# Optimization experiments

Measured on AMD Instinct MI355X. Metric: run time of the kernel, lower is better.

Reference implementation:

```python
import jax, jax.numpy as jnp
import numpy as np

# Binary (sign) weight linear: y = x @ sign(W)^T + b

def _binarize(w):
    # sign with sign(0) mapped to +1, as in typical BinaryLinear impls
    return jnp.where(w >= 0, 1.0, -1.0).astype(w.dtype)

def setup_inputs() -> dict:
    key = jax.random.key(0)
    ks = jax.random.split(key, 7)
    B = 65536
    x = jax.random.normal(ks[0], (B, 28, 28), dtype=jnp.float32)
    W1 = jax.random.normal(ks[1], (1000, 784), dtype=jnp.float32) * 0.05
    b1 = jax.random.normal(ks[2], (1000,), dtype=jnp.float32) * 0.01
    W2 = jax.random.normal(ks[3], (500, 1000), dtype=jnp.float32) * 0.05
    b2 = jax.random.normal(ks[4], (500,), dtype=jnp.float32) * 0.01
    W3 = jax.random.normal(ks[5], (10, 500), dtype=jnp.float32) * 0.05
    b3 = jax.random.normal(ks[6], (10,), dtype=jnp.float32) * 0.01
    return {"x": x, "W1": W1, "b1": b1, "W2": W2, "b2": b2, "W3": W3, "b3": b3}

def reference(x, W1, b1, W2, b2, W3, b3):
    h = x.reshape(x.shape[0], -1)                      # [B, 784]
    h = jnp.maximum(h @ _binarize(W1).T + b1, 0.0)     # [B, 1000]
    h = jnp.maximum(h @ _binarize(W2).T + b2, 0.0)     # [B, 500]
    return h @ _binarize(W3).T + b3                    # [B, 10]
```

## Files before the change

### kernel.cpp

```cpp
#include <hip/hip_runtime.h>
#include <stdint.h>


typedef __attribute__((ext_vector_type(8))) short bf16x8;
typedef __attribute__((ext_vector_type(4))) float f32x4;

typedef const __attribute__((address_space(1))) unsigned int* as1_u32p;
typedef __attribute__((address_space(3))) unsigned int* as3_u32p;

__device__ __forceinline__ void glds16(const void* g, void* l) {
  __builtin_amdgcn_global_load_lds((as1_u32p)g, (as3_u32p)l, 16, 0, 0);
}

__device__ __forceinline__ unsigned short f2bf(float f) {
  union { float f; unsigned u; } c;
  c.f = f;
  unsigned u = c.u;
  u += 0x7FFFu + ((u >> 16) & 1u);
  return (unsigned short)(u >> 16);
}

__global__ void binarize_kernel(const float* __restrict__ src, int Ns, int Ks,
                                short* __restrict__ dst, int Np, int Kp) {
  int idx = blockIdx.x * 256 + threadIdx.x;
  if (idx >= Np * Kp) return;
  int n = idx / Kp;
  int k = idx - n * Kp;
  short v = 0;
  if (n < Ns && k < Ks)
    v = (src[n * Ks + k] >= 0.0f) ? (short)0x3F80 : (short)0xBF80;
  dst[idx] = v;
}

__global__ void convert_x_kernel(const float* __restrict__ X, short* __restrict__ Xp) {
  const int g = blockIdx.x * 256 + threadIdx.x;
  if (g >= 65536 * 100) return;
  const int row = g / 100;
  const int c = (g - row * 100) * 8;
  short tmp[8];
  if (c < 784) {
    const float* s = X + (size_t)row * 784 + c;
    float4 f0 = *(const float4*)s;
    float4 f1 = *(const float4*)(s + 4);
    tmp[0] = (short)f2bf(f0.x); tmp[1] = (short)f2bf(f0.y);
    tmp[2] = (short)f2bf(f0.z); tmp[3] = (short)f2bf(f0.w);
    tmp[4] = (short)f2bf(f1.x); tmp[5] = (short)f2bf(f1.y);
    tmp[6] = (short)f2bf(f1.z); tmp[7] = (short)f2bf(f1.w);
  } else {
#pragma unroll
    for (int i = 0; i < 8; ++i) tmp[i] = 0;
  }
  *(bf16x8*)(Xp + (size_t)row * 800 + c) = *(bf16x8*)(tmp);
}

template <int KP, int NP, int NR>
__global__ __launch_bounds__(256, 2)
void gemm_bb(const short* __restrict__ A, const short* __restrict__ Wb,
             const float* __restrict__ bias, short* __restrict__ Hout) {
  __shared__ short As[128 * 32];
  __shared__ short Bs[128 * 32];

  const int tid = threadIdx.x;
  const int lane = tid & 63;
  const int wave = tid >> 6;
  const int wm = wave >> 1, wn = wave & 1;
  const int l15 = lane & 15;
  const int quad = lane >> 4;
  const int m0 = blockIdx.y * 128;
  const int n0 = blockIdx.x * 128;

  const int sr = wave * 16 + (lane >> 2);
  const int sks = (lane & 3) * 8;
  const short* asrc = A + (size_t)(m0 + sr) * KP + sks;
  const short* bsrc = Wb + (size_t)(n0 + sr) * KP + sks;
  short* adst = As + (wave * 16) * 32;
  short* bdst = Bs + (wave * 16) * 32;

  f32x4 acc[4][4];
#pragma unroll
  for (int i = 0; i < 4; ++i)
#pragma unroll
    for (int j = 0; j < 4; ++j) acc[i][j] = (f32x4){0.f, 0.f, 0.f, 0.f};

  for (int k0 = 0; k0 < KP; k0 += 32) {
    glds16(asrc + k0, adst);
    glds16(asrc + k0 + (size_t)64 * KP, adst + 64 * 32);
    glds16(bsrc + k0, bdst);
    glds16(bsrc + k0 + (size_t)64 * KP, bdst + 64 * 32);
    __syncthreads();

    const short* abase = As + (size_t)(wm * 64 + l15) * 32 + quad * 8;
    const short* bbase = Bs + (size_t)(wn * 64 + l15) * 32 + quad * 8;
    bf16x8 af[4], bfr[4];
#pragma unroll
    for (int i = 0; i < 4; ++i) af[i] = *(const bf16x8*)(abase + i * 16 * 32);
#pragma unroll
    for (int j = 0; j < 4; ++j) bfr[j] = *(const bf16x8*)(bbase + j * 16 * 32);
#pragma unroll
    for (int i = 0; i < 4; ++i)
#pragma unroll
      for (int j = 0; j < 4; ++j)
        acc[i][j] = __builtin_amdgcn_mfma_f32_16x16x32_bf16(af[i], bfr[j], acc[i][j], 0, 0, 0);
    __syncthreads();
  }

#pragma unroll
  for (int j = 0; j < 4; ++j) {
    const int n = n0 + wn * 64 + j * 16 + l15;
    const float bv = (n < NR) ? bias[n] : 0.f;
#pragma unroll
    for (int i = 0; i < 4; ++i) {
      const int mr = m0 + wm * 64 + i * 16 + quad * 4;
#pragma unroll
      for (int r = 0; r < 4; ++r) {
        float v = acc[i][j][r] + bv;
        v = v > 0.f ? v : 0.f;
        Hout[(size_t)(mr + r) * NP + n] = (short)f2bf(v);
      }
    }
  }
}

__global__ __launch_bounds__(256, 2)
void gemm1_fused_kernel(const float* __restrict__ X, const short* __restrict__ Wb,
                        const float* __restrict__ bias, short* __restrict__ H) {
  constexpr int K = 784, KP = 800, NP = 1024, NR = 1000;
  __shared__ short As[128 * 32];
  __shared__ short Bs[128 * 32];

  const int tid = threadIdx.x;
  const int lane = tid & 63;
  const int wave = tid >> 6;
  const int wm = wave >> 1, wn = wave & 1;
  const int l15 = lane & 15;
  const int quad = lane >> 4;
  const int m0 = blockIdx.y * 128;
  const int n0 = blockIdx.x * 128;

  const int ar = tid >> 1;
  const int aks = (tid & 1) * 16;
  const float* xrow = X + (size_t)(m0 + ar) * K;
  short* adst = As + ar * 32 + aks;

  const int br = wave * 16 + (lane >> 2);
  const int bks = (lane & 3) * 8;
  const short* brow0 = Wb + (size_t)(n0 + br) * KP + bks;
  short* bdst = Bs + (wave * 16) * 32;

  f32x4 acc[4][4];
#pragma unroll
  for (int i = 0; i < 4; ++i)
#pragma unroll
    for (int j = 0; j < 4; ++j) acc[i][j] = (f32x4){0.f, 0.f, 0.f, 0.f};

  for (int k0 = 0; k0 < KP; k0 += 32) {
    glds16(brow0 + k0, bdst);
    glds16(brow0 + k0 + (size_t)64 * KP, bdst + 64 * 32);
    short tmp[16];
#pragma unroll
    for (int c = 0; c < 4; ++c) {
      const int kk = k0 + aks + c * 4;
      float4 f;
      if (kk < K)
        f = *(const float4*)(xrow + kk);
      else
        f = make_float4(0.f, 0.f, 0.f, 0.f);
      tmp[c * 4 + 0] = (short)f2bf(f.x);
      tmp[c * 4 + 1] = (short)f2bf(f.y);
      tmp[c * 4 + 2] = (short)f2bf(f.z);
      tmp[c * 4 + 3] = (short)f2bf(f.w);
    }
    *(bf16x8*)(adst) = *(bf16x8*)(tmp);
    *(bf16x8*)(adst + 8) = *(bf16x8*)(tmp + 8);

    __syncthreads();

    const short* abase = As + (size_t)(wm * 64 + l15) * 32 + quad * 8;
    const short* bbase = Bs + (size_t)(wn * 64 + l15) * 32 + quad * 8;
    bf16x8 af[4], bfr[4];
#pragma unroll
    for (int i = 0; i < 4; ++i) af[i] = *(const bf16x8*)(abase + i * 16 * 32);
#pragma unroll
    for (int j = 0; j < 4; ++j) bfr[j] = *(const bf16x8*)(bbase + j * 16 * 32);
#pragma unroll
    for (int i = 0; i < 4; ++i)
#pragma unroll
      for (int j = 0; j < 4; ++j)
        acc[i][j] = __builtin_amdgcn_mfma_f32_16x16x32_bf16(af[i], bfr[j], acc[i][j], 0, 0, 0);
    __syncthreads();
  }

#pragma unroll
  for (int j = 0; j < 4; ++j) {
    const int n = n0 + wn * 64 + j * 16 + l15;
    const float bv = (n < NR) ? bias[n] : 0.f;
#pragma unroll
    for (int i = 0; i < 4; ++i) {
      const int mr = m0 + wm * 64 + i * 16 + quad * 4;
#pragma unroll
      for (int r = 0; r < 4; ++r) {
        float v = acc[i][j][r] + bv;
        v = v > 0.f ? v : 0.f;
        H[(size_t)(mr + r) * NP + n] = (short)f2bf(v);
      }
    }
  }
}

__global__ __launch_bounds__(256, 2)
void gemm3_kernel(const short* __restrict__ Hin, const short* __restrict__ Wb,
                  const float* __restrict__ bias, float* __restrict__ Out) {
  constexpr int KP = 512;
  constexpr int BSTRIDE = 520;
  __shared__ short As[128 * 32];
  __shared__ short Bs[16 * BSTRIDE];

  const int tid = threadIdx.x;
  const int lane = tid & 63;
  const int wave = tid >> 6;
  const int l15 = lane & 15;
  const int quad = lane >> 4;
  const int m0 = blockIdx.x * 128;

  for (int t = tid; t < 16 * 512 / 8; t += 256) {
    int n = (t * 8) / 512;
    int k = (t * 8) % 512;
    *(bf16x8*)(Bs + n * BSTRIDE + k) = *(const bf16x8*)(Wb + t * 8);
  }

  const int sr = wave * 16 + (lane >> 2);
  const int sks = (lane & 3) * 8;
  const short* arow0 = Hin + (size_t)(m0 + sr) * KP + sks;
  short* adst = As + (wave * 16) * 32;

  f32x4 acc[2];
#pragma unroll
  for (int i = 0; i < 2; ++i) acc[i] = (f32x4){0.f, 0.f, 0.f, 0.f};

  for (int k0 = 0; k0 < KP; k0 += 32) {
    glds16(arow0 + k0, adst);
    glds16(arow0 + k0 + (size_t)64 * KP, adst + 64 * 32);
    __syncthreads();

    bf16x8 bfr = *(const bf16x8*)(Bs + l15 * BSTRIDE + k0 + quad * 8);
#pragma unroll
    for (int i = 0; i < 2; ++i) {
      bf16x8 af = *(const bf16x8*)(As + (size_t)(wave * 32 + i * 16 + l15) * 32 + quad * 8);
      acc[i] = __builtin_amdgcn_mfma_f32_16x16x32_bf16(af, bfr, acc[i], 0, 0, 0);
    }
    __syncthreads();
  }

  if (l15 < 10) {
    const float bv = bias[l15];
#pragma unroll
    for (int i = 0; i < 2; ++i)
#pragma unroll
      for (int r = 0; r < 4; ++r) {
        const int mr = m0 + wave * 32 + i * 16 + quad * 4 + r;
        Out[(size_t)mr * 10 + l15] = acc[i][r] + bv;
      }
  }
}

extern "C" void kernel_launch(void* const* d_in, const int* in_sizes, int n_in,
                              void* d_out, int out_size, void* d_ws, size_t ws_size,
                              hipStream_t stream) {
  const float* x = (const float*)d_in[0];
  const float* W1 = (const float*)d_in[1];
  const float* b1 = (const float*)d_in[2];
  const float* W2 = (const float*)d_in[3];
  const float* b2 = (const float*)d_in[4];
  const float* W3 = (const float*)d_in[5];
  const float* b3 = (const float*)d_in[6];
  float* out = (float*)d_out;

  const size_t szW1 = (size_t)1024 * 800 * 2;
  const size_t szW2 = (size_t)512 * 1024 * 2;
  const size_t szW3 = (size_t)16 * 512 * 2;
  const size_t szH1 = (size_t)65536 * 1024 * 2;
  const size_t szXp = (size_t)65536 * 800 * 2;
  const size_t need = szW1 + szW2 + szW3 + szH1 + szXp;

  uint8_t* p = (uint8_t*)d_ws;
  short* W1b = (short*)p; p += szW1;
  short* W2b = (short*)p; p += szW2;
  short* W3b = (short*)p; p += szW3;
  short* h1 = (short*)p; p += szH1;
  short* Z = (short*)p;

  binarize_kernel<<<(1024 * 800 + 255) / 256, 256, 0, stream>>>(W1, 1000, 784, W1b, 1024, 800);
  binarize_kernel<<<(512 * 1024 + 255) / 256, 256, 0, stream>>>(W2, 500, 1000, W2b, 512, 1024);
  binarize_kernel<<<(16 * 512 + 255) / 256, 256, 0, stream>>>(W3, 10, 500, W3b, 16, 512);

  if (ws_size >= need) {
    short* Xp = Z;
    short* h2 = Z;
    convert_x_kernel<<<(65536 * 100 + 255) / 256, 256, 0, stream>>>(x, Xp);
    gemm_bb<800, 1024, 1000><<<dim3(8, 512), 256, 0, stream>>>(Xp, W1b, b1, h1);
    gemm_bb<1024, 512, 500><<<dim3(4, 512), 256, 0, stream>>>(h1, W2b, b2, h2);
    gemm3_kernel<<<512, 256, 0, stream>>>(h2, W3b, b3, out);
  } else {
    short* h2 = Z;
    gemm1_fused_kernel<<<dim3(8, 512), 256, 0, stream>>>(x, W1b, b1, h1);
    gemm_bb<1024, 512, 500><<<dim3(4, 512), 256, 0, stream>>>(h1, W2b, b2, h2);
    gemm3_kernel<<<512, 256, 0, stream>>>(h2, W3b, b3, out);
  }
}
```

Measured before the change: 612.9 us.

## Use BK=64 GEMM tiles with XCD-aware block mapping and rotated K start

Replaces the BK=32 GEMM with a BK=64 variant that loads two 32-wide K slices per sync, halving the barrier count per tile. Blocks are remapped so each XCD covers a contiguous band of M rows, and each N-column block starts its K loop at a rotated offset to spread concurrent reads across memory. K padding for layer 1 grows to 832 to fit 64-wide steps. The final 10-output GEMM is rewritten to hold all W3 fragments in registers and stage a full 64x512 A tile in one pass. The cost is more LDS per block and wasted MACs on the extra padding.

```diff
diff --git a/kernel.cpp b/kernel.cpp
--- a/kernel.cpp
+++ b/kernel.cpp
@@ -34,9 +34,9 @@
 
 __global__ void convert_x_kernel(const float* __restrict__ X, short* __restrict__ Xp) {
   const int g = blockIdx.x * 256 + threadIdx.x;
-  if (g >= 65536 * 100) return;
-  const int row = g / 100;
-  const int c = (g - row * 100) * 8;
+  if (g >= 65536 * 104) return;
+  const int row = g / 104;
+  const int c = (g - row * 104) * 8;
   short tmp[8];
   if (c < 784) {
     const float* s = X + (size_t)row * 784 + c;
@@ -50,13 +50,100 @@
 #pragma unroll
     for (int i = 0; i < 8; ++i) tmp[i] = 0;
   }
-  *(bf16x8*)(Xp + (size_t)row * 800 + c) = *(bf16x8*)(tmp);
-}
-
-template <int KP, int NP, int NR>
+  *(bf16x8*)(Xp + (size_t)row * 832 + c) = *(bf16x8*)(tmp);
+}
+
+template <int KP, int NIT, int NP, int NR, int GLOG>
 __global__ __launch_bounds__(256, 2)
-void gemm_bb(const short* __restrict__ A, const short* __restrict__ Wb,
-             const float* __restrict__ bias, short* __restrict__ Hout) {
+void gemm_bk64(const short* __restrict__ A, const short* __restrict__ Wb,
+               const float* __restrict__ bias, short* __restrict__ Hout) {
+  __shared__ short As0[128 * 32];
+  __shared__ short As1[128 * 32];
+  __shared__ short Bs0[128 * 32];
+  __shared__ short Bs1[128 * 32];
+
+  const int d = blockIdx.x;
+  const int xcd = d & 7;
+  const int slot = d >> 3;
+  const int j = slot & ((1 << GLOG) - 1);
+  const int m0 = ((xcd << 6) + (slot >> GLOG)) * 128;
+  const int n0 = j * 128;
+  const int start = (j * NIT) >> GLOG;
+
+  const int tid = threadIdx.x;
+  const int lane = tid & 63;
+  const int wave = tid >> 6;
+  const int wm = wave >> 1, wn = wave & 1;
+  const int l15 = lane & 15;
+  const int quad = lane >> 4;
+
+  const int sr = wave * 16 + (lane >> 2);
+  const int sks = (lane & 3) * 8;
+  const short* asrc = A + (size_t)(m0 + sr) * KP + sks;
+  const short* bsrc = Wb + (size_t)(n0 + sr) * KP + sks;
+  const int sdst = (wave * 16) * 32;
+
+  f32x4 acc[4][4];
+#pragma unroll
+  for (int i = 0; i < 4; ++i)
+#pragma unroll
+    for (int j2 = 0; j2 < 4; ++j2) acc[i][j2] = (f32x4){0.f, 0.f, 0.f, 0.f};
+
+  for (int it = 0; it < NIT; ++it) {
+    int kit = start + it;
+    if (kit >= NIT) kit -= NIT;
+    const int k0 = kit * 64;
+
+    glds16(asrc + k0, As0 + sdst);
+    glds16(asrc + k0 + (size_t)64 * KP, As0 + sdst + 64 * 32);
+    glds16(asrc + k0 + 32, As1 + sdst);
+    glds16(asrc + k0 + 32 + (size_t)64 * KP, As1 + sdst + 64 * 32);
+    glds16(bsrc + k0, Bs0 + sdst);
+    glds16(bsrc + k0 + (size_t)64 * KP, Bs0 + sdst + 64 * 32);
+    glds16(bsrc + k0 + 32, Bs1 + sdst);
+    glds16(bsrc + k0 + 32 + (size_t)64 * KP, Bs1 + sdst + 64 * 32);
+    __syncthreads();
+
+#pragma unroll
+    for (int h = 0; h < 2; ++h) {
+      const short* As = h ? As1 : Bs0 - 128 * 32;
+      const short* ab = (h ? As1 : As0) + (wm * 64 + l15) * 32 + quad * 8;
+      const short* bb = (h ? Bs1 : Bs0) + (wn * 64 + l15) * 32 + quad * 8;
+      bf16x8 af[4], bfr[4];
+#pragma unroll
+      for (int i = 0; i < 4; ++i) af[i] = *(const bf16x8*)(ab + i * 16 * 32);
+#pragma unroll
+      for (int j2 = 0; j2 < 4; ++j2) bfr[j2] = *(const bf16x8*)(bb + j2 * 16 * 32);
+#pragma unroll
+      for (int i = 0; i < 4; ++i)
+#pragma unroll
+        for (int j2 = 0; j2 < 4; ++j2)
+          acc[i][j2] = __builtin_amdgcn_mfma_f32_16x16x32_bf16(af[i], bfr[j2], acc[i][j2], 0, 0, 0);
+    }
+    __syncthreads();
+  }
+
+#pragma unroll
+  for (int j2 = 0; j2 < 4; ++j2) {
+    const int n = n0 + wn * 64 + j2 * 16 + l15;
+    const float bv = (n < NR) ? bias[n] : 0.f;
+#pragma unroll
+    for (int i = 0; i < 4; ++i) {
+      const int mr = m0 + wm * 64 + i * 16 + quad * 4;
+#pragma unroll
+      for (int r = 0; r < 4; ++r) {
+        float v = acc[i][j2][r] + bv;
+        v = v > 0.f ? v : 0.f;
+        Hout[(size_t)(mr + r) * NP + n] = (short)f2bf(v);
+      }
+    }
+  }
+}
+
+__global__ __launch_bounds__(256, 2)
+void gemm1_fused_kernel(const float* __restrict__ X, const short* __restrict__ Wb,
+                        const float* __restrict__ bias, short* __restrict__ H) {
+  constexpr int K = 784, KP = 832, NP = 1024, NR = 1000;
   __shared__ short As[128 * 32];
   __shared__ short Bs[128 * 32];
 
@@ -69,74 +156,6 @@
   const int m0 = blockIdx.y * 128;
   const int n0 = blockIdx.x * 128;
 
-  const int sr = wave * 16 + (lane >> 2);
-  const int sks = (lane & 3) * 8;
-  const short* asrc = A + (size_t)(m0 + sr) * KP + sks;
-  const short* bsrc = Wb + (size_t)(n0 + sr) * KP + sks;
-  short* adst = As + (wave * 16) * 32;
-  short* bdst = Bs + (wave * 16) * 32;
-
-  f32x4 acc[4][4];
-#pragma unroll
-  for (int i = 0; i < 4; ++i)
-#pragma unroll
-    for (int j = 0; j < 4; ++j) acc[i][j] = (f32x4){0.f, 0.f, 0.f, 0.f};
-
-  for (int k0 = 0; k0 < KP; k0 += 32) {
-    glds16(asrc + k0, adst);
-    glds16(asrc + k0 + (size_t)64 * KP, adst + 64 * 32);
-    glds16(bsrc + k0, bdst);
-    glds16(bsrc + k0 + (size_t)64 * KP, bdst + 64 * 32);
-    __syncthreads();
-
-    const short* abase = As + (size_t)(wm * 64 + l15) * 32 + quad * 8;
-    const short* bbase = Bs + (size_t)(wn * 64 + l15) * 32 + quad * 8;
-    bf16x8 af[4], bfr[4];
-#pragma unroll
-    for (int i = 0; i < 4; ++i) af[i] = *(const bf16x8*)(abase + i * 16 * 32);
-#pragma unroll
-    for (int j = 0; j < 4; ++j) bfr[j] = *(const bf16x8*)(bbase + j * 16 * 32);
-#pragma unroll
-    for (int i = 0; i < 4; ++i)
-#pragma unroll
-      for (int j = 0; j < 4; ++j)
-        acc[i][j] = __builtin_amdgcn_mfma_f32_16x16x32_bf16(af[i], bfr[j], acc[i][j], 0, 0, 0);
-    __syncthreads();
-  }
-
-#pragma unroll
-  for (int j = 0; j < 4; ++j) {
-    const int n = n0 + wn * 64 + j * 16 + l15;
-    const float bv = (n < NR) ? bias[n] : 0.f;
-#pragma unroll
-    for (int i = 0; i < 4; ++i) {
-      const int mr = m0 + wm * 64 + i * 16 + quad * 4;
-#pragma unroll
-      for (int r = 0; r < 4; ++r) {
-        float v = acc[i][j][r] + bv;
-        v = v > 0.f ? v : 0.f;
-        Hout[(size_t)(mr + r) * NP + n] = (short)f2bf(v);
-      }
-    }
-  }
-}
-
-__global__ __launch_bounds__(256, 2)
-void gemm1_fused_kernel(const float* __restrict__ X, const short* __restrict__ Wb,
-                        const float* __restrict__ bias, short* __restrict__ H) {
-  constexpr int K = 784, KP = 800, NP = 1024, NR = 1000;
-  __shared__ short As[128 * 32];
-  __shared__ short Bs[128 * 32];
-
-  const int tid = threadIdx.x;
-  const int lane = tid & 63;
-  const int wave = tid >> 6;
-  const int wm = wave >> 1, wn = wave & 1;
-  const int l15 = lane & 15;
-  const int quad = lane >> 4;
-  const int m0 = blockIdx.y * 128;
-  const int n0 = blockIdx.x * 128;
-
   const int ar = tid >> 1;
   const int aks = (tid & 1) * 16;
   const float* xrow = X + (size_t)(m0 + ar) * K;
@@ -151,7 +170,7 @@
 #pragma unroll
   for (int i = 0; i < 4; ++i)
 #pragma unroll
-    for (int j = 0; j < 4; ++j) acc[i][j] = (f32x4){0.f, 0.f, 0.f, 0.f};
+    for (int j2 = 0; j2 < 4; ++j2) acc[i][j2] = (f32x4){0.f, 0.f, 0.f, 0.f};
 
   for (int k0 = 0; k0 < KP; k0 += 32) {
     glds16(brow0 + k0, bdst);
@@ -161,7 +180,7 @@
     for (int c = 0; c < 4; ++c) {
       const int kk = k0 + aks + c * 4;
       float4 f;
-      if (kk < K)
+      if (kk + 3 < K)
         f = *(const float4*)(xrow + kk);
       else
         f = make_float4(0.f, 0.f, 0.f, 0.f);
@@ -172,7 +191,6 @@
     }
     *(bf16x8*)(adst) = *(bf16x8*)(tmp);
     *(bf16x8*)(adst + 8) = *(bf16x8*)(tmp + 8);
-
     __syncthreads();
 
     const short* abase = As + (size_t)(wm * 64 + l15) * 32 + quad * 8;
@@ -181,25 +199,25 @@
 #pragma unroll
     for (int i = 0; i < 4; ++i) af[i] = *(const bf16x8*)(abase + i * 16 * 32);
 #pragma unroll
-    for (int j = 0; j < 4; ++j) bfr[j] = *(const bf16x8*)(bbase + j * 16 * 32);
+    for (int j2 = 0; j2 < 4; ++j2) bfr[j2] = *(const bf16x8*)(bbase + j2 * 16 * 32);
 #pragma unroll
     for (int i = 0; i < 4; ++i)
 #pragma unroll
-      for (int j = 0; j < 4; ++j)
-        acc[i][j] = __builtin_amdgcn_mfma_f32_16x16x32_bf16(af[i], bfr[j], acc[i][j], 0, 0, 0);
+      for (int j2 = 0; j2 < 4; ++j2)
+        acc[i][j2] = __builtin_amdgcn_mfma_f32_16x16x32_bf16(af[i], bfr[j2], acc[i][j2], 0, 0, 0);
     __syncthreads();
   }
 
 #pragma unroll
-  for (int j = 0; j < 4; ++j) {
-    const int n = n0 + wn * 64 + j * 16 + l15;
+  for (int j2 = 0; j2 < 4; ++j2) {
+    const int n = n0 + wn * 64 + j2 * 16 + l15;
     const float bv = (n < NR) ? bias[n] : 0.f;
 #pragma unroll
     for (int i = 0; i < 4; ++i) {
       const int mr = m0 + wm * 64 + i * 16 + quad * 4;
 #pragma unroll
       for (int r = 0; r < 4; ++r) {
-        float v = acc[i][j][r] + bv;
+        float v = acc[i][j2][r] + bv;
         v = v > 0.f ? v : 0.f;
         H[(size_t)(mr + r) * NP + n] = (short)f2bf(v);
       }
@@ -211,55 +229,43 @@
 void gemm3_kernel(const short* __restrict__ Hin, const short* __restrict__ Wb,
                   const float* __restrict__ bias, float* __restrict__ Out) {
   constexpr int KP = 512;
-  constexpr int BSTRIDE = 520;
-  __shared__ short As[128 * 32];
-  __shared__ short Bs[16 * BSTRIDE];
+  __shared__ short As[64 * KP];
 
   const int tid = threadIdx.x;
   const int lane = tid & 63;
   const int wave = tid >> 6;
   const int l15 = lane & 15;
   const int quad = lane >> 4;
-  const int m0 = blockIdx.x * 128;
-
-  for (int t = tid; t < 16 * 512 / 8; t += 256) {
-    int n = (t * 8) / 512;
-    int k = (t * 8) % 512;
-    *(bf16x8*)(Bs + n * BSTRIDE + k) = *(const bf16x8*)(Wb + t * 8);
-  }
-
-  const int sr = wave * 16 + (lane >> 2);
-  const int sks = (lane & 3) * 8;
-  const short* arow0 = Hin + (size_t)(m0 + sr) * KP + sks;
-  short* adst = As + (wave * 16) * 32;
-
-  f32x4 acc[2];
-#pragma unroll
-  for (int i = 0; i < 2; ++i) acc[i] = (f32x4){0.f, 0.f, 0.f, 0.f};
-
-  for (int k0 = 0; k0 < KP; k0 += 32) {
-    glds16(arow0 + k0, adst);
-    glds16(arow0 + k0 + (size_t)64 * KP, adst + 64 * 32);
-    __syncthreads();
-
-    bf16x8 bfr = *(const bf16x8*)(Bs + l15 * BSTRIDE + k0 + quad * 8);
-#pragma unroll
-    for (int i = 0; i < 2; ++i) {
-      bf16x8 af = *(const bf16x8*)(As + (size_t)(wave * 32 + i * 16 + l15) * 32 + quad * 8);
-      acc[i] = __builtin_amdgcn_mfma_f32_16x16x32_bf16(af, bfr, acc[i], 0, 0, 0);
-    }
-    __syncthreads();
+  const int m0 = blockIdx.x * 64;
+
+  bf16x8 bw[16];
+#pragma unroll
+  for (int kk = 0; kk < 16; ++kk)
+    bw[kk] = *(const bf16x8*)(Wb + l15 * KP + kk * 32 + quad * 8);
+
+  const short* asrc = Hin + (size_t)(m0 + wave * 16) * KP + lane * 8;
+  short* adst = As + (size_t)(wave * 16) * KP;
+#pragma unroll
+  for (int t = 0; t < 16; ++t)
+    glds16(asrc + (size_t)t * KP, adst + (size_t)t * KP);
+
+  __syncthreads();
+
+  f32x4 acc = (f32x4){0.f, 0.f, 0.f, 0.f};
+  const short* abase = As + (size_t)(wave * 16 + l15) * KP + quad * 8;
+#pragma unroll
+  for (int kk = 0; kk < 16; ++kk) {
+    bf16x8 af = *(const bf16x8*)(abase + kk * 32);
+    acc = __builtin_amdgcn_mfma_f32_16x16x32_bf16(af, bw[kk], acc, 0, 0, 0);
   }
 
   if (l15 < 10) {
     const float bv = bias[l15];
 #pragma unroll
-    for (int i = 0; i < 2; ++i)
-#pragma unroll
-      for (int r = 0; r < 4; ++r) {
-        const int mr = m0 + wave * 32 + i * 16 + quad * 4 + r;
-        Out[(size_t)mr * 10 + l15] = acc[i][r] + bv;
-      }
+    for (int r = 0; r < 4; ++r) {
+      const int mr = m0 + wave * 16 + quad * 4 + r;
+      Out[(size_t)mr * 10 + l15] = acc[r] + bv;
+    }
   }
 }
 
@@ -275,11 +281,11 @@
   const float* b3 = (const float*)d_in[6];
   float* out = (float*)d_out;
 
-  const size_t szW1 = (size_t)1024 * 800 * 2;
+  const size_t szW1 = (size_t)1024 * 832 * 2;
   const size_t szW2 = (size_t)512 * 1024 * 2;
   const size_t szW3 = (size_t)16 * 512 * 2;
   const size_t szH1 = (size_t)65536 * 1024 * 2;
-  const size_t szXp = (size_t)65536 * 800 * 2;
+  const size_t szXp = (size_t)65536 * 832 * 2;
   const size_t need = szW1 + szW2 + szW3 + szH1 + szXp;
 
   uint8_t* p = (uint8_t*)d_ws;
@@ -289,21 +295,21 @@
   short* h1 = (short*)p; p += szH1;
   short* Z = (short*)p;
 
-  binarize_kernel<<<(1024 * 800 + 255) / 256, 256, 0, stream>>>(W1, 1000, 784, W1b, 1024, 800);
+  binarize_kernel<<<(1024 * 832 + 255) / 256, 256, 0, stream>>>(W1, 1000, 784, W1b, 1024, 832);
   binarize_kernel<<<(512 * 1024 + 255) / 256, 256, 0, stream>>>(W2, 500, 1000, W2b, 512, 1024);
   binarize_kernel<<<(16 * 512 + 255) / 256, 256, 0, stream>>>(W3, 10, 500, W3b, 16, 512);
 
   if (ws_size >= need) {
     short* Xp = Z;
     short* h2 = Z;
-    convert_x_kernel<<<(65536 * 100 + 255) / 256, 256, 0, stream>>>(x, Xp);
-    gemm_bb<800, 1024, 1000><<<dim3(8, 512), 256, 0, stream>>>(Xp, W1b, b1, h1);
-    gemm_bb<1024, 512, 500><<<dim3(4, 512), 256, 0, stream>>>(h1, W2b, b2, h2);
-    gemm3_kernel<<<512, 256, 0, stream>>>(h2, W3b, b3, out);
+    convert_x_kernel<<<(65536 * 104 + 255) / 256, 256, 0, stream>>>(x, Xp);
+    gemm_bk64<832, 13, 1024, 1000, 3><<<4096, 256, 0, stream>>>(Xp, W1b, b1, h1);
+    gemm_bk64<1024, 16, 512, 500, 2><<<2048, 256, 0, stream>>>(h1, W2b, b2, h2);
+    gemm3_kernel<<<1024, 256, 0, stream>>>(h2, W3b, b3, out);
   } else {
     short* h2 = Z;
     gemm1_fused_kernel<<<dim3(8, 512), 256, 0, stream>>>(x, W1b, b1, h1);
-    gemm_bb<1024, 512, 500><<<dim3(4, 512), 256, 0, stream>>>(h1, W2b, b2, h2);
-    gemm3_kernel<<<512, 256, 0, stream>>>(h2, W3b, b3, out);
-  }
-}
+    gemm_bk64<1024, 16, 512, 500, 2><<<2048, 256, 0, stream>>>(h1, W2b, b2, h2);
+    gemm3_kernel<<<1024, 256, 0, stream>>>(h2, W3b, b3, out);
+  }
+}
```

Result: faster. 575.8 us (-6.0%).
